# Performance work log

Hardware: AMD Instinct MI355X
Metric: run time of the kernel (lower is better)

Reference implementation:

```python
import jax, jax.numpy as jnp
import numpy as np

LN_EPS = 1e-12
BIG = 1e30
BAND = 15  # end index may be at most 15 tokens after start


def output_layer(x, w1, b1, g, b, w2, b2):
    # Linear -> ReLU -> LayerNorm -> Linear (dropout is identity at eval)
    h = jax.nn.relu(x @ w1 + b1)
    mu = jnp.mean(h, axis=-1, keepdims=True)
    var = jnp.mean(jnp.square(h - mu), axis=-1, keepdims=True)
    h = (h - mu) * jax.lax.rsqrt(var + LN_EPS) * g + b
    return h @ w2 + b2


def setup_inputs() -> dict:
    key = jax.random.key(0)
    ks = jax.random.split(key, 8)
    B, S, D = 8, 4096, 1024
    H2 = 2 * D
    inp = {
        "context_input": jax.random.normal(ks[0], (B, S, D), jnp.float32),
        "context_mask": jnp.ones((B, S), jnp.float32),
    }
    def head(k1, k2, n_ans):
        return (
            0.02 * jax.random.normal(k1, (D, H2), jnp.float32),
            jnp.zeros((H2,), jnp.float32),
            jnp.ones((H2,), jnp.float32),
            jnp.zeros((H2,), jnp.float32),
            0.02 * jax.random.normal(k2, (H2, n_ans), jnp.float32),
            jnp.zeros((n_ans,), jnp.float32),
        )
    for name, k1, k2, n_ans in [("start", ks[1], ks[2], 1), ("end", ks[3], ks[4], 1), ("type", ks[5], ks[6], 4)]:
        w1, b1, g, b, w2, b2 = head(k1, k2, n_ans)
        inp[f"{name}_w1"] = w1; inp[f"{name}_b1"] = b1
        inp[f"{name}_g"] = g; inp[f"{name}_b"] = b
        inp[f"{name}_w2"] = w2; inp[f"{name}_b2"] = b2
    return inp


def reference(context_input, context_mask,
              start_w1, start_b1, start_g, start_b, start_w2, start_b2,
              end_w1, end_b1, end_g, end_b, end_w2, end_b2,
              type_w1, type_b1, type_g, type_b, type_w2, type_b2):
    S = context_input.shape[1]
    start_pred = output_layer(context_input, start_w1, start_b1, start_g, start_b, start_w2, start_b2)[..., 0] \
        - BIG * (1.0 - context_mask)  # [B,S]
    end_pred = output_layer(context_input, end_w1, end_b1, end_g, end_b, end_w2, end_b2)[..., 0] \
        - BIG * (1.0 - context_mask)  # [B,S]
    type_pred = output_layer(context_input[:, 0, :], type_w1, type_b1, type_g, type_b, type_w2, type_b2)  # [B,4]

    # outer[b,i,j] = start[b,i] + end[b,j], masked to band 0 <= j-i <= 15
    outer = start_pred[:, :, None] + end_pred[:, None, :]  # [B,S,S]
    i = jnp.arange(S)[:, None]
    j = jnp.arange(S)[None, :]
    band = ((j >= i) & (j <= i + BAND)).astype(outer.dtype)  # [S,S]
    outer = outer - BIG * (1.0 - band)[None]

    yp1 = jnp.argmax(jnp.max(outer, axis=2), axis=1)  # best start index [B]
    yp2 = jnp.argmax(jnp.max(outer, axis=1), axis=1)  # best end index [B]
    return start_pred, end_pred, type_pred, yp1, yp2
```

## Files before the change

kernel.cpp:

```cpp
#include <hip/hip_runtime.h>

typedef _Float16 f16x8 __attribute__((ext_vector_type(8)));
typedef float f32x4 __attribute__((ext_vector_type(4)));

#define BIGF 1e30f
#define M_TOT 32768
#define H2 2048

#define WS_XH 0u
#define WS_WT 67108864u
#define WS_BVEC 75497472u
#define WS_GW2 75513856u
#define WS_CONSTS 75530240u
#define WS_PART 75530496u
#define WS_TPART 100696320u

__global__ void k_convert_x(const float* __restrict__ x, _Float16* __restrict__ xh) {
  size_t i = ((size_t)blockIdx.x * 256 + threadIdx.x) * 8;
  float4 v0 = *(const float4*)(x + i);
  float4 v1 = *(const float4*)(x + i + 4);
  f16x8 h;
  h[0] = (_Float16)v0.x; h[1] = (_Float16)v0.y; h[2] = (_Float16)v0.z; h[3] = (_Float16)v0.w;
  h[4] = (_Float16)v1.x; h[5] = (_Float16)v1.y; h[6] = (_Float16)v1.z; h[7] = (_Float16)v1.w;
  *(f16x8*)(xh + i) = h;
}

__global__ void k_convert_w(const float* __restrict__ w_s, const float* __restrict__ w_e,
                            _Float16* __restrict__ wt) {
  __shared__ float tile[64][65];
  const float* w = blockIdx.z ? w_e : w_s;
  int n0 = blockIdx.x * 64, k0 = blockIdx.y * 64;
  int tx = threadIdx.x & 63, ty = threadIdx.x >> 6;
#pragma unroll
  for (int i = ty; i < 64; i += 4) tile[i][tx] = w[(size_t)(k0 + i) * H2 + n0 + tx];
  __syncthreads();
#pragma unroll
  for (int i = ty; i < 64; i += 4) {
    wt[((size_t)(blockIdx.z * H2 + n0 + i)) * 1024 + k0 + tx] = (_Float16)tile[tx][i];
  }
}

__global__ void k_prep(const float* __restrict__ s_b1, const float* __restrict__ s_g,
                       const float* __restrict__ s_w2, const float* __restrict__ s_b,
                       const float* __restrict__ s_b2, const float* __restrict__ e_b1,
                       const float* __restrict__ e_g, const float* __restrict__ e_w2,
                       const float* __restrict__ e_b, const float* __restrict__ e_b2,
                       float* __restrict__ bvec, float* __restrict__ gw2,
                       float* __restrict__ consts) {
  int blk = blockIdx.x;
  if (blk < 16) {
    int i = blk * 256 + threadIdx.x;
    int head = i >> 11, j = i & (H2 - 1);
    bvec[i] = head ? e_b1[j] : s_b1[j];
    gw2[i] = head ? e_g[j] * e_w2[j] : s_g[j] * s_w2[j];
  } else {
    int h = blk - 16;
    const float* g = h ? e_g : s_g;
    const float* b = h ? e_b : s_b;
    const float* w2 = h ? e_w2 : s_w2;
    const float* b2 = h ? e_b2 : s_b2;
    float c1 = 0.f, c2 = 0.f;
    for (int j = threadIdx.x; j < H2; j += 256) {
      float w = w2[j];
      c1 += g[j] * w;
      c2 += b[j] * w;
    }
    for (int m = 1; m < 64; m <<= 1) { c1 += __shfl_xor(c1, m); c2 += __shfl_xor(c2, m); }
    __shared__ float r1[4], r2[4];
    int wid = threadIdx.x >> 6;
    if ((threadIdx.x & 63) == 0) { r1[wid] = c1; r2[wid] = c2; }
    __syncthreads();
    if (threadIdx.x == 0) {
      consts[h * 2 + 0] = r1[0] + r1[1] + r1[2] + r1[3];
      consts[h * 2 + 1] = r2[0] + r2[1] + r2[2] + r2[3] + b2[0];
    }
  }
}

#define BUF 65536u
#define STA(q, tile, bufo)                                                              \
  __builtin_amdgcn_global_load_lds(                                                     \
      (const __attribute__((address_space(1))) unsigned int*)(srcA + (size_t)(q) * 131072 + (size_t)(tile) * 128), \
      (__attribute__((address_space(3))) unsigned int*)(lds + (bufo) + (q) * 8192 + t * 16), 16, 0, 0)
#define STB(q, tile, bufo)                                                              \
  __builtin_amdgcn_global_load_lds(                                                     \
      (const __attribute__((address_space(1))) unsigned int*)(srcB + (size_t)(q) * 131072 + (size_t)(tile) * 128), \
      (__attribute__((address_space(3))) unsigned int*)(lds + (bufo) + 32768u + (q) * 8192 + t * 16), 16, 0, 0)

#define RD_B(kh)                                                                        \
  _Pragma("unroll")                                                                     \
  for (int nj = 0; nj < 4; ++nj)                                                        \
    bf[nj] = *(const f16x8*)(lds + ob + 32768u +                                        \
                             (unsigned)((wn + nj * 16 + c15) * 128) +                   \
                             (unsigned)((((kh) * 64) + g4 * 16) ^ xorv));

#define RD_A(mh, kh)                                                                    \
  _Pragma("unroll")                                                                     \
  for (int i = 0; i < 4; ++i)                                                           \
    af[i] = *(const f16x8*)(lds + ob +                                                  \
                            (unsigned)((wmg * 128 + (mh) * 64 + i * 16 + c15) * 128) +  \
                            (unsigned)((((kh) * 64) + g4 * 16) ^ xorv));

#define PH_TAIL                                                                         \
  __builtin_amdgcn_sched_barrier(0);                                                    \
  __builtin_amdgcn_s_barrier();                                                         \
  asm volatile("s_waitcnt lgkmcnt(0)" ::: "memory");                                    \
  __builtin_amdgcn_sched_barrier(0);

#define BAR2                                                                            \
  __builtin_amdgcn_sched_barrier(0);                                                    \
  __builtin_amdgcn_s_barrier();                                                         \
  __builtin_amdgcn_sched_barrier(0);

#define MF16(mh)                                                                        \
  __builtin_amdgcn_s_setprio(1);                                                        \
  _Pragma("unroll")                                                                     \
  for (int i = 0; i < 4; ++i)                                                           \
    _Pragma("unroll")                                                                   \
    for (int nj = 0; nj < 4; ++nj)                                                      \
      acc[(mh) * 4 + i][nj] =                                                           \
          __builtin_amdgcn_mfma_f32_16x16x32_f16(af[i], bf[nj], acc[(mh) * 4 + i][nj], 0, 0, 0); \
  __builtin_amdgcn_s_setprio(0);

__global__ __launch_bounds__(512, 2) void k_gemm(const _Float16* __restrict__ Xh,
                                                 const _Float16* __restrict__ Wt,
                                                 const float* __restrict__ bvec,
                                                 const float* __restrict__ gw2,
                                                 float* __restrict__ partials) {
  __shared__ char lds[2 * BUF];
  const int bid = blockIdx.x;
  const int swzb = (bid & 7) * 256 + (bid >> 3);
  const int nb = swzb & 15;
  const int mb = swzb >> 4;
  const int t = threadIdx.x;
  const int lane = t & 63, wid = t >> 6;
  const int c15 = lane & 15, g4 = lane >> 4;
  const int wmg = wid >> 2;
  const int wn = (wid & 3) * 64;

  f32x4 acc[8][4];
#pragma unroll
  for (int i = 0; i < 8; ++i)
#pragma unroll
    for (int j = 0; j < 4; ++j) acc[i][j] = (f32x4){0.f, 0.f, 0.f, 0.f};

  const char* Abase = (const char*)(Xh + (size_t)mb * 256 * 1024);
  const char* Bbase = (const char*)(Wt + (size_t)nb * 256 * 1024);
  const int rowl = t >> 3;
  const int swz = ((t & 7) * 16) ^ ((rowl & 7) << 4);
  const char* srcA = Abase + (size_t)rowl * 2048 + swz;
  const char* srcB = Bbase + (size_t)rowl * 2048 + swz;

  const int xorv = (c15 & 7) << 4;

  STA(0, 0, 0); STA(1, 0, 0); STA(2, 0, 0); STA(3, 0, 0);
  STB(0, 0, 0); STB(1, 0, 0); STB(2, 0, 0); STB(3, 0, 0);
  STB(0, 1, BUF); STB(1, 1, BUF); STB(2, 1, BUF); STB(3, 1, BUF);
  STA(0, 1, BUF); STA(2, 1, BUF);
  asm volatile("s_waitcnt vmcnt(6)" ::: "memory");
  __builtin_amdgcn_s_barrier();
  __builtin_amdgcn_sched_barrier(0);

  f16x8 af[4], bf[4];

#pragma unroll
  for (int g = 0; g < 16; ++g) {
    const unsigned ob = (unsigned)(g & 1) * BUF;
    const unsigned on = ob ^ BUF;

    if (g < 15) { STA(1, g + 1, on); STA(3, g + 1, on); }
    RD_B(0); RD_A(0, 0);
    PH_TAIL
    MF16(0)
    BAR2

    RD_A(1, 0);
    PH_TAIL
    MF16(1)
    BAR2

    RD_B(1); RD_A(0, 1);
    PH_TAIL
    MF16(0)
    BAR2

    if (g < 14) {
      STB(0, g + 2, ob); STB(1, g + 2, ob); STB(2, g + 2, ob); STB(3, g + 2, ob);
      STA(0, g + 2, ob); STA(2, g + 2, ob);
    }
    RD_A(1, 1);
    PH_TAIL
    MF16(1)
    __builtin_amdgcn_sched_barrier(0);
    if (g < 14)       asm volatile("s_waitcnt vmcnt(6)" ::: "memory");
    else if (g == 14) asm volatile("s_waitcnt vmcnt(0)" ::: "memory");
    __builtin_amdgcn_s_barrier();
    __builtin_amdgcn_sched_barrier(0);
  }

  float bv[4], gv[4];
#pragma unroll
  for (int nj = 0; nj < 4; ++nj) {
    int col = nb * 256 + wn + nj * 16 + c15;
    bv[nj] = bvec[col];
    gv[nj] = gw2[col];
  }
  const int slice = nb * 4 + (wid & 3);
#pragma unroll
  for (int mi = 0; mi < 8; ++mi) {
#pragma unroll
    for (int r = 0; r < 4; ++r) {
      float s1 = 0.f, s2 = 0.f, s3 = 0.f;
#pragma unroll
      for (int nj = 0; nj < 4; ++nj) {
        float v = acc[mi][nj][r] + bv[nj];
        v = fmaxf(v, 0.f);
        s1 += v;
        s2 += v * v;
        s3 += v * gv[nj];
      }
#pragma unroll
      for (int m = 1; m < 16; m <<= 1) {
        s1 += __shfl_xor(s1, m);
        s2 += __shfl_xor(s2, m);
        s3 += __shfl_xor(s3, m);
      }
      if (c15 == 0) {
        int rowg = mb * 256 + wmg * 128 + mi * 16 + g4 * 4 + r;
        partials[((size_t)(slice * 3 + 0)) * M_TOT + rowg] = s1;
        partials[((size_t)(slice * 3 + 1)) * M_TOT + rowg] = s2;
        partials[((size_t)(slice * 3 + 2)) * M_TOT + rowg] = s3;
      }
    }
  }
}

__global__ void k_reduce(const float* __restrict__ partials, const float* __restrict__ consts,
                         const float* __restrict__ mask, float* __restrict__ out) {
  int m = blockIdx.x * 256 + threadIdx.x;
  float s1 = 0.f, s2 = 0.f, s3 = 0.f, e1 = 0.f, e2 = 0.f, e3 = 0.f;
  for (int nb2 = 0; nb2 < 32; ++nb2) {
    s1 += partials[((size_t)(nb2 * 3 + 0)) * M_TOT + m];
    s2 += partials[((size_t)(nb2 * 3 + 1)) * M_TOT + m];
    s3 += partials[((size_t)(nb2 * 3 + 2)) * M_TOT + m];
  }
  for (int nb2 = 32; nb2 < 64; ++nb2) {
    e1 += partials[((size_t)(nb2 * 3 + 0)) * M_TOT + m];
    e2 += partials[((size_t)(nb2 * 3 + 1)) * M_TOT + m];
    e3 += partials[((size_t)(nb2 * 3 + 2)) * M_TOT + m];
  }
  const float H = (float)H2;
  float mu = s1 / H;
  float var = fmaxf(s2 / H - mu * mu, 0.f);
  float rs = 1.f / sqrtf(var + 1e-12f);
  float score_s = rs * (s3 - mu * consts[0]) + consts[1];
  mu = e1 / H;
  var = fmaxf(e2 / H - mu * mu, 0.f);
  rs = 1.f / sqrtf(var + 1e-12f);
  float score_e = rs * (e3 - mu * consts[2]) + consts[3];
  float mk = BIGF * (1.f - mask[m]);
  out[m] = score_s - mk;
  out[M_TOT + m] = score_e - mk;
}

__global__ void k_type_partial(const float* __restrict__ X, const float* __restrict__ w1,
                               const float* __restrict__ b1, const float* __restrict__ g,
                               const float* __restrict__ w2, float* __restrict__ tpart) {
  __shared__ float xs[1024];
  int cb = blockIdx.x, tok = blockIdx.y, t = threadIdx.x;
  const float* xp = X + (size_t)tok * 4096 * 1024;
  for (int i = t; i < 1024; i += 256) xs[i] = xp[i];
  __syncthreads();
  int j = cb * 256 + t;
  float dot = 0.f;
  for (int k = 0; k < 1024; ++k) dot += xs[k] * w1[(size_t)k * H2 + j];
  float h = fmaxf(dot + b1[j], 0.f);
  float gj = g[j];
  float s[6];
  s[0] = h;
  s[1] = h * h;
#pragma unroll
  for (int c = 0; c < 4; ++c) s[2 + c] = h * gj * w2[j * 4 + c];
  for (int m = 1; m < 64; m <<= 1)
#pragma unroll
    for (int q = 0; q < 6; ++q) s[q] += __shfl_xor(s[q], m);
  __shared__ float red[4][6];
  int wid = t >> 6;
  if ((t & 63) == 0)
#pragma unroll
    for (int q = 0; q < 6; ++q) red[wid][q] = s[q];
  __syncthreads();
  if (t == 0)
#pragma unroll
    for (int q = 0; q < 6; ++q)
      tpart[(tok * 8 + cb) * 6 + q] = red[0][q] + red[1][q] + red[2][q] + red[3][q];
}

__global__ void k_type_final(const float* __restrict__ tpart, const float* __restrict__ g,
                             const float* __restrict__ bb, const float* __restrict__ w2,
                             const float* __restrict__ b2, float* __restrict__ out) {
  int t = threadIdx.x;
  float c1[4] = {0.f, 0.f, 0.f, 0.f}, c2[4] = {0.f, 0.f, 0.f, 0.f};
  for (int j = t; j < H2; j += 256) {
    float gj = g[j], bj = bb[j];
#pragma unroll
    for (int c = 0; c < 4; ++c) {
      float w = w2[j * 4 + c];
      c1[c] += gj * w;
      c2[c] += bj * w;
    }
  }
  for (int m = 1; m < 64; m <<= 1)
#pragma unroll
    for (int c = 0; c < 4; ++c) { c1[c] += __shfl_xor(c1[c], m); c2[c] += __shfl_xor(c2[c], m); }
  __shared__ float rC1[4][4], rC2[4][4];
  int wid = t >> 6;
  if ((t & 63) == 0)
#pragma unroll
    for (int c = 0; c < 4; ++c) { rC1[wid][c] = c1[c]; rC2[wid][c] = c2[c]; }
  __syncthreads();
  __shared__ float sC1[4], sC2[4];
  if (t < 4) {
    sC1[t] = rC1[0][t] + rC1[1][t] + rC1[2][t] + rC1[3][t];
    sC2[t] = rC2[0][t] + rC2[1][t] + rC2[2][t] + rC2[3][t];
  }
  __syncthreads();
  if (t < 32) {
    int tok = t >> 2, c = t & 3;
    float s1 = 0.f, s2 = 0.f, s3 = 0.f;
    for (int cb = 0; cb < 8; ++cb) {
      s1 += tpart[(tok * 8 + cb) * 6 + 0];
      s2 += tpart[(tok * 8 + cb) * 6 + 1];
      s3 += tpart[(tok * 8 + cb) * 6 + 2 + c];
    }
    float mu = s1 / (float)H2;
    float var = fmaxf(s2 / (float)H2 - mu * mu, 0.f);
    float rs = 1.f / sqrtf(var + 1e-12f);
    out[65536 + tok * 4 + c] = rs * (s3 - mu * sC1[c]) + sC2[c] + b2[c];
  }
}

__global__ void k_band(const float* __restrict__ preds, float* __restrict__ out) {
  __shared__ float ss[4096], se[4096];
  int b = blockIdx.x, t = threadIdx.x;
  for (int i = t; i < 4096; i += 256) {
    ss[i] = preds[(size_t)b * 4096 + i];
    se[i] = preds[M_TOT + (size_t)b * 4096 + i];
  }
  __syncthreads();
  float bv1 = -3.0e38f, bv2 = -3.0e38f;
  int bi1 = 0x7fffffff, bi2 = 0x7fffffff;
  for (int i = t; i < 4096; i += 256) {
    float m1 = -3.0e38f;
    int jmax = i + 15 < 4095 ? i + 15 : 4095;
    for (int j = i; j <= jmax; ++j) m1 = fmaxf(m1, se[j]);
    float v1 = ss[i] + m1;
    if (v1 > bv1 || (v1 == bv1 && i < bi1)) { bv1 = v1; bi1 = i; }
    float m2 = -3.0e38f;
    int imin = i - 15 > 0 ? i - 15 : 0;
    for (int j = imin; j <= i; ++j) m2 = fmaxf(m2, ss[j]);
    float v2 = se[i] + m2;
    if (v2 > bv2 || (v2 == bv2 && i < bi2)) { bv2 = v2; bi2 = i; }
  }
  for (int m = 1; m < 64; m <<= 1) {
    float ov = __shfl_xor(bv1, m);
    int oi = __shfl_xor(bi1, m);
    if (ov > bv1 || (ov == bv1 && oi < bi1)) { bv1 = ov; bi1 = oi; }
    ov = __shfl_xor(bv2, m);
    oi = __shfl_xor(bi2, m);
    if (ov > bv2 || (ov == bv2 && oi < bi2)) { bv2 = ov; bi2 = oi; }
  }
  __shared__ float rv[2][4];
  __shared__ int ri[2][4];
  int wid = t >> 6;
  if ((t & 63) == 0) { rv[0][wid] = bv1; ri[0][wid] = bi1; rv[1][wid] = bv2; ri[1][wid] = bi2; }
  __syncthreads();
  if (t == 0) {
    float v = rv[0][0];
    int ix = ri[0][0];
    for (int w = 1; w < 4; ++w)
      if (rv[0][w] > v || (rv[0][w] == v && ri[0][w] < ix)) { v = rv[0][w]; ix = ri[0][w]; }
    out[65568 + b] = (float)ix;
    v = rv[1][0];
    ix = ri[1][0];
    for (int w = 1; w < 4; ++w)
      if (rv[1][w] > v || (rv[1][w] == v && ri[1][w] < ix)) { v = rv[1][w]; ix = ri[1][w]; }
    out[65576 + b] = (float)ix;
  }
}

extern "C" void kernel_launch(void* const* d_in, const int* in_sizes, int n_in, void* d_out,
                              int out_size, void* d_ws, size_t ws_size, hipStream_t stream) {
  const float* X = (const float*)d_in[0];
  const float* mask = (const float*)d_in[1];
  const float* s_w1 = (const float*)d_in[2];
  const float* s_b1 = (const float*)d_in[3];
  const float* s_g = (const float*)d_in[4];
  const float* s_b = (const float*)d_in[5];
  const float* s_w2 = (const float*)d_in[6];
  const float* s_b2 = (const float*)d_in[7];
  const float* e_w1 = (const float*)d_in[8];
  const float* e_b1 = (const float*)d_in[9];
  const float* e_g = (const float*)d_in[10];
  const float* e_b = (const float*)d_in[11];
  const float* e_w2 = (const float*)d_in[12];
  const float* e_b2 = (const float*)d_in[13];
  const float* t_w1 = (const float*)d_in[14];
  const float* t_b1 = (const float*)d_in[15];
  const float* t_g = (const float*)d_in[16];
  const float* t_b = (const float*)d_in[17];
  const float* t_w2 = (const float*)d_in[18];
  const float* t_b2 = (const float*)d_in[19];

  char* ws = (char*)d_ws;
  _Float16* Xh = (_Float16*)(ws + WS_XH);
  _Float16* Wt = (_Float16*)(ws + WS_WT);
  float* bvec = (float*)(ws + WS_BVEC);
  float* gw2 = (float*)(ws + WS_GW2);
  float* consts = (float*)(ws + WS_CONSTS);
  float* partials = (float*)(ws + WS_PART);
  float* tpart = (float*)(ws + WS_TPART);
  float* out = (float*)d_out;

  k_convert_x<<<16384, 256, 0, stream>>>(X, Xh);
  k_convert_w<<<dim3(32, 16, 2), 256, 0, stream>>>(s_w1, e_w1, Wt);
  k_prep<<<18, 256, 0, stream>>>(s_b1, s_g, s_w2, s_b, s_b2, e_b1, e_g, e_w2, e_b, e_b2,
                                 bvec, gw2, consts);
  k_gemm<<<2048, 512, 0, stream>>>(Xh, Wt, bvec, gw2, partials);
  k_reduce<<<128, 256, 0, stream>>>(partials, consts, mask, out);
  k_type_partial<<<dim3(8, 8), 256, 0, stream>>>(X, t_w1, t_b1, t_g, t_w2, tpart);
  k_type_final<<<1, 256, 0, stream>>>(tpart, t_g, t_b, t_w2, t_b2, out);
  k_band<<<8, 256, 0, stream>>>(out, out);
}
```

Measured before the change: 430.5 us.

## Shrink GEMM tile to 256x128 with single-buffered LDS and in-block partial reduction

The fused GEMM tile drops from 256x256 to 256x128, and the double-buffered 128KB LDS pipeline becomes a 48KB single buffer with a full vmcnt(0) wait and barrier after each k-step. Launch bounds rise to 4 blocks per SM, and the grid becomes 32x128 in plain 2D order with no L2-friendly block swizzle. The two column-half waves' LayerNorm partials are summed in LDS before writing, so the reduce kernel reads 16 slices per head instead of 32. This aims for higher occupancy and less partial traffic, but global loads no longer overlap compute inside a block, and each A tile is now reloaded twice as often.

```diff
diff --git a/kernel.cpp b/kernel.cpp
--- a/kernel.cpp
+++ b/kernel.cpp
@@ -77,29 +77,22 @@
   }
 }
 
-#define BUF 65536u
-#define STA(q, tile, bufo)                                                              \
+#define STA(q, tile)                                                                    \
   __builtin_amdgcn_global_load_lds(                                                     \
       (const __attribute__((address_space(1))) unsigned int*)(srcA + (size_t)(q) * 131072 + (size_t)(tile) * 128), \
-      (__attribute__((address_space(3))) unsigned int*)(lds + (bufo) + (q) * 8192 + t * 16), 16, 0, 0)
-#define STB(q, tile, bufo)                                                              \
+      (__attribute__((address_space(3))) unsigned int*)(lds + (q) * 8192 + t * 16), 16, 0, 0)
+#define STB(q, tile)                                                                    \
   __builtin_amdgcn_global_load_lds(                                                     \
       (const __attribute__((address_space(1))) unsigned int*)(srcB + (size_t)(q) * 131072 + (size_t)(tile) * 128), \
-      (__attribute__((address_space(3))) unsigned int*)(lds + (bufo) + 32768u + (q) * 8192 + t * 16), 16, 0, 0)
-
-#define RD_B(kh)                                                                        \
+      (__attribute__((address_space(3))) unsigned int*)(lds + 32768 + (q) * 8192 + t * 16), 16, 0, 0)
+
+#define RD_AB(low)                                                                      \
+  _Pragma("unroll")                                                                     \
+  for (int i = 0; i < 4; ++i)                                                           \
+    af[i] = *(const f16x8*)(lds + arow + i * 2048 + (low));                             \
   _Pragma("unroll")                                                                     \
   for (int nj = 0; nj < 4; ++nj)                                                        \
-    bf[nj] = *(const f16x8*)(lds + ob + 32768u +                                        \
-                             (unsigned)((wn + nj * 16 + c15) * 128) +                   \
-                             (unsigned)((((kh) * 64) + g4 * 16) ^ xorv));
-
-#define RD_A(mh, kh)                                                                    \
-  _Pragma("unroll")                                                                     \
-  for (int i = 0; i < 4; ++i)                                                           \
-    af[i] = *(const f16x8*)(lds + ob +                                                  \
-                            (unsigned)((wmg * 128 + (mh) * 64 + i * 16 + c15) * 128) +  \
-                            (unsigned)((((kh) * 64) + g4 * 16) ^ xorv));
+    bf[nj] = *(const f16x8*)(lds + brow + nj * 2048 + (low));
 
 #define PH_TAIL                                                                         \
   __builtin_amdgcn_sched_barrier(0);                                                    \
@@ -112,52 +105,52 @@
   __builtin_amdgcn_s_barrier();                                                         \
   __builtin_amdgcn_sched_barrier(0);
 
-#define MF16(mh)                                                                        \
+#define MF16                                                                            \
   __builtin_amdgcn_s_setprio(1);                                                        \
   _Pragma("unroll")                                                                     \
   for (int i = 0; i < 4; ++i)                                                           \
     _Pragma("unroll")                                                                   \
     for (int nj = 0; nj < 4; ++nj)                                                      \
-      acc[(mh) * 4 + i][nj] =                                                           \
-          __builtin_amdgcn_mfma_f32_16x16x32_f16(af[i], bf[nj], acc[(mh) * 4 + i][nj], 0, 0, 0); \
+      acc[i][nj] = __builtin_amdgcn_mfma_f32_16x16x32_f16(af[i], bf[nj], acc[i][nj], 0, 0, 0); \
   __builtin_amdgcn_s_setprio(0);
 
-__global__ __launch_bounds__(512, 2) void k_gemm(const _Float16* __restrict__ Xh,
+__global__ __launch_bounds__(512, 4) void k_gemm(const _Float16* __restrict__ Xh,
                                                  const _Float16* __restrict__ Wt,
                                                  const float* __restrict__ bvec,
                                                  const float* __restrict__ gw2,
                                                  float* __restrict__ partials) {
-  __shared__ char lds[2 * BUF];
-  const int bid = blockIdx.x;
-  const int swzb = (bid & 7) * 256 + (bid >> 3);
-  const int nb = swzb & 15;
-  const int mb = swzb >> 4;
+  __shared__ char lds[49152];
+  const int nb = blockIdx.x;
+  const int mb = blockIdx.y;
   const int t = threadIdx.x;
   const int lane = t & 63, wid = t >> 6;
   const int c15 = lane & 15, g4 = lane >> 4;
-  const int wmg = wid >> 2;
-  const int wn = (wid & 3) * 64;
-
-  f32x4 acc[8][4];
-#pragma unroll
-  for (int i = 0; i < 8; ++i)
+  const int wmg = wid >> 1;
+  const int wq = wid & 1;
+  const int wn = wq * 64;
+
+  f32x4 acc[4][4];
+#pragma unroll
+  for (int i = 0; i < 4; ++i)
 #pragma unroll
     for (int j = 0; j < 4; ++j) acc[i][j] = (f32x4){0.f, 0.f, 0.f, 0.f};
 
   const char* Abase = (const char*)(Xh + (size_t)mb * 256 * 1024);
-  const char* Bbase = (const char*)(Wt + (size_t)nb * 256 * 1024);
+  const char* Bbase = (const char*)(Wt + (size_t)nb * 128 * 1024);
   const int rowl = t >> 3;
   const int swz = ((t & 7) * 16) ^ ((rowl & 7) << 4);
   const char* srcA = Abase + (size_t)rowl * 2048 + swz;
   const char* srcB = Bbase + (size_t)rowl * 2048 + swz;
 
   const int xorv = (c15 & 7) << 4;
-
-  STA(0, 0, 0); STA(1, 0, 0); STA(2, 0, 0); STA(3, 0, 0);
-  STB(0, 0, 0); STB(1, 0, 0); STB(2, 0, 0); STB(3, 0, 0);
-  STB(0, 1, BUF); STB(1, 1, BUF); STB(2, 1, BUF); STB(3, 1, BUF);
-  STA(0, 1, BUF); STA(2, 1, BUF);
-  asm volatile("s_waitcnt vmcnt(6)" ::: "memory");
+  const int low0 = (g4 * 16) ^ xorv;
+  const int low1 = (64 + g4 * 16) ^ xorv;
+  const int arow = (wmg * 64 + c15) * 128;
+  const int brow = 32768 + (wn + c15) * 128;
+
+  STA(0, 0); STA(1, 0); STA(2, 0); STA(3, 0);
+  STB(0, 0); STB(1, 0);
+  asm volatile("s_waitcnt vmcnt(0)" ::: "memory");
   __builtin_amdgcn_s_barrier();
   __builtin_amdgcn_sched_barrier(0);
 
@@ -165,49 +158,35 @@
 
 #pragma unroll
   for (int g = 0; g < 16; ++g) {
-    const unsigned ob = (unsigned)(g & 1) * BUF;
-    const unsigned on = ob ^ BUF;
-
-    if (g < 15) { STA(1, g + 1, on); STA(3, g + 1, on); }
-    RD_B(0); RD_A(0, 0);
+    RD_AB(low0)
     PH_TAIL
-    MF16(0)
+    MF16
     BAR2
-
-    RD_A(1, 0);
+    RD_AB(low1)
     PH_TAIL
-    MF16(1)
+    MF16
     BAR2
-
-    RD_B(1); RD_A(0, 1);
-    PH_TAIL
-    MF16(0)
-    BAR2
-
-    if (g < 14) {
-      STB(0, g + 2, ob); STB(1, g + 2, ob); STB(2, g + 2, ob); STB(3, g + 2, ob);
-      STA(0, g + 2, ob); STA(2, g + 2, ob);
-    }
-    RD_A(1, 1);
-    PH_TAIL
-    MF16(1)
-    __builtin_amdgcn_sched_barrier(0);
-    if (g < 14)       asm volatile("s_waitcnt vmcnt(6)" ::: "memory");
-    else if (g == 14) asm volatile("s_waitcnt vmcnt(0)" ::: "memory");
-    __builtin_amdgcn_s_barrier();
-    __builtin_amdgcn_sched_barrier(0);
-  }
+    if (g < 15) {
+      STA(0, g + 1); STA(1, g + 1); STA(2, g + 1); STA(3, g + 1);
+      STB(0, g + 1); STB(1, g + 1);
+      asm volatile("s_waitcnt vmcnt(0)" ::: "memory");
+      __builtin_amdgcn_s_barrier();
+      __builtin_amdgcn_sched_barrier(0);
+    }
+  }
+
+  __syncthreads();
+  float* red = (float*)lds;
 
   float bv[4], gv[4];
 #pragma unroll
   for (int nj = 0; nj < 4; ++nj) {
-    int col = nb * 256 + wn + nj * 16 + c15;
+    int col = nb * 128 + wn + nj * 16 + c15;
     bv[nj] = bvec[col];
     gv[nj] = gw2[col];
   }
-  const int slice = nb * 4 + (wid & 3);
-#pragma unroll
-  for (int mi = 0; mi < 8; ++mi) {
+#pragma unroll
+  for (int mi = 0; mi < 4; ++mi) {
 #pragma unroll
     for (int r = 0; r < 4; ++r) {
       float s1 = 0.f, s2 = 0.f, s3 = 0.f;
@@ -226,12 +205,21 @@
         s3 += __shfl_xor(s3, m);
       }
       if (c15 == 0) {
-        int rowg = mb * 256 + wmg * 128 + mi * 16 + g4 * 4 + r;
-        partials[((size_t)(slice * 3 + 0)) * M_TOT + rowg] = s1;
-        partials[((size_t)(slice * 3 + 1)) * M_TOT + rowg] = s2;
-        partials[((size_t)(slice * 3 + 2)) * M_TOT + rowg] = s3;
+        int row = mi * 16 + g4 * 4 + r;
+        float* p = red + (((wmg * 2 + wq) * 64 + row) * 3);
+        p[0] = s1; p[1] = s2; p[2] = s3;
       }
     }
+  }
+  __syncthreads();
+  for (int idx = t; idx < 768; idx += 512) {
+    int wmgi = idx / 192;
+    int rem = idx - wmgi * 192;
+    int row = rem / 3, k = rem - row * 3;
+    float s = red[((wmgi * 2 + 0) * 64 + row) * 3 + k] +
+              red[((wmgi * 2 + 1) * 64 + row) * 3 + k];
+    int rowg = mb * 256 + wmgi * 64 + row;
+    partials[((size_t)(nb * 3 + k)) * M_TOT + rowg] = s;
   }
 }
 
@@ -239,15 +227,15 @@
                          const float* __restrict__ mask, float* __restrict__ out) {
   int m = blockIdx.x * 256 + threadIdx.x;
   float s1 = 0.f, s2 = 0.f, s3 = 0.f, e1 = 0.f, e2 = 0.f, e3 = 0.f;
-  for (int nb2 = 0; nb2 < 32; ++nb2) {
-    s1 += partials[((size_t)(nb2 * 3 + 0)) * M_TOT + m];
-    s2 += partials[((size_t)(nb2 * 3 + 1)) * M_TOT + m];
-    s3 += partials[((size_t)(nb2 * 3 + 2)) * M_TOT + m];
-  }
-  for (int nb2 = 32; nb2 < 64; ++nb2) {
-    e1 += partials[((size_t)(nb2 * 3 + 0)) * M_TOT + m];
-    e2 += partials[((size_t)(nb2 * 3 + 1)) * M_TOT + m];
-    e3 += partials[((size_t)(nb2 * 3 + 2)) * M_TOT + m];
+  for (int nb = 0; nb < 16; ++nb) {
+    s1 += partials[((size_t)(nb * 3 + 0)) * M_TOT + m];
+    s2 += partials[((size_t)(nb * 3 + 1)) * M_TOT + m];
+    s3 += partials[((size_t)(nb * 3 + 2)) * M_TOT + m];
+  }
+  for (int nb = 16; nb < 32; ++nb) {
+    e1 += partials[((size_t)(nb * 3 + 0)) * M_TOT + m];
+    e2 += partials[((size_t)(nb * 3 + 1)) * M_TOT + m];
+    e3 += partials[((size_t)(nb * 3 + 2)) * M_TOT + m];
   }
   const float H = (float)H2;
   float mu = s1 / H;
@@ -426,7 +414,7 @@
   k_convert_w<<<dim3(32, 16, 2), 256, 0, stream>>>(s_w1, e_w1, Wt);
   k_prep<<<18, 256, 0, stream>>>(s_b1, s_g, s_w2, s_b, s_b2, e_b1, e_g, e_w2, e_b, e_b2,
                                  bvec, gw2, consts);
-  k_gemm<<<2048, 512, 0, stream>>>(Xh, Wt, bvec, gw2, partials);
+  k_gemm<<<dim3(32, 128), 512, 0, stream>>>(Xh, Wt, bvec, gw2, partials);
   k_reduce<<<128, 256, 0, stream>>>(partials, consts, mask, out);
   k_type_partial<<<dim3(8, 8), 256, 0, stream>>>(X, t_w1, t_b1, t_g, t_w2, tpart);
   k_type_final<<<1, 256, 0, stream>>>(tpart, t_g, t_b, t_w2, t_b2, out);
```

Result: slower. 454.6 us (+5.6%).
